# Performance work log

Hardware: AMD Instinct MI355X
Metric: run time of the kernel (lower is better)

## Reference

```python
import jax, jax.numpy as jnp
import numpy as np

# module hyperparameters (init kwargs)
D_MODEL = 1024
NUM_HEADS = 16
D_K = D_MODEL // NUM_HEADS
WINDOW_SIZE = 256
GLOBAL_TOKENS = 64
SEQ_LEN = 4096
BATCH = 1
NEG_INF = float('-inf')


def build_local_window_mask(seq_len, window_size, global_tokens):
    # 0 where attention is allowed, -inf where blocked
    i = jnp.arange(seq_len)[:, None]
    j = jnp.arange(seq_len)[None, :]
    allowed = (i < global_tokens) | (j < global_tokens) | (jnp.abs(i - j) <= window_size)
    return jnp.where(allowed, 0.0, NEG_INF).astype(jnp.float32)


def setup_inputs() -> dict:
    key = jax.random.key(0)
    ks = jax.random.split(key, 12)
    s = 1.0 / np.sqrt(D_MODEL)
    inp = {
        'q': jax.random.normal(ks[0], (BATCH, SEQ_LEN, D_MODEL), jnp.float32),
        'k': jax.random.normal(ks[1], (BATCH, SEQ_LEN, D_MODEL), jnp.float32),
        'v': jax.random.normal(ks[2], (BATCH, SEQ_LEN, D_MODEL), jnp.float32),
        # nn.Linear weights: shape (out, in), applied as x @ W.T + b
        'w_q': jax.random.normal(ks[3], (D_MODEL, D_MODEL), jnp.float32) * s,
        'b_q': jax.random.normal(ks[4], (D_MODEL,), jnp.float32) * s,
        'w_k': jax.random.normal(ks[5], (D_MODEL, D_MODEL), jnp.float32) * s,
        'b_k': jax.random.normal(ks[6], (D_MODEL,), jnp.float32) * s,
        'w_v': jax.random.normal(ks[7], (D_MODEL, D_MODEL), jnp.float32) * s,
        'b_v': jax.random.normal(ks[8], (D_MODEL,), jnp.float32) * s,
        'w_o': jax.random.normal(ks[9], (D_MODEL, D_MODEL), jnp.float32) * s,
        'b_o': jax.random.normal(ks[10], (D_MODEL,), jnp.float32) * s,
    }
    return inp


def reference(q, k, v, w_q, b_q, w_k, b_k, w_v, b_v, w_o, b_o):
    B, S, _ = q.shape
    scale = 1.0 / np.sqrt(D_K)

    def proj(x, w, b):  # (B,S,D) -> (B,H,S,Dk)
        y = x @ w.T + b
        return y.reshape(B, S, NUM_HEADS, D_K).transpose(0, 2, 1, 3)

    Q = proj(q, w_q, b_q)
    K = proj(k, w_k, b_k)
    V = proj(v, w_v, b_v)

    local_mask = build_local_window_mask(S, WINDOW_SIZE, GLOBAL_TOKENS)  # (S,S)
    scores = jnp.einsum('bhqd,bhkd->bhqk', Q, K) * scale + local_mask[None, None]
    attn = jax.nn.softmax(scores, axis=-1)
    out = jnp.einsum('bhqk,bhkd->bhqd', attn, V)  # (B,H,S,Dk)
    out = out.transpose(0, 2, 1, 3).reshape(B, S, D_MODEL)
    return out @ w_o.T + b_o
```

## Files before the change

kernel.cpp:

```cpp
#include <hip/hip_runtime.h>

#define S_LEN 4096
#define DMODEL 1024
#define NHEADS 16
#define DKH 64
#define WIN 256
#define GTOK 64
#define NSPLIT 8

typedef unsigned short u16t;
typedef __attribute__((ext_vector_type(8))) short short8;
typedef __attribute__((ext_vector_type(4))) float f32x4;

__device__ __forceinline__ u16t f2bf(float x) {
  union { float f; unsigned int u; } v; v.f = x;
  unsigned int r = v.u + 0x7FFFu + ((v.u >> 16) & 1u);
  return (u16t)(r >> 16);
}

__device__ __forceinline__ unsigned int cvtpk(float lo, float hi) {
  unsigned int r;
  asm("v_cvt_pk_bf16_f32 %0, %1, %2" : "=v"(r) : "v"(lo), "v"(hi));
  return r;
}

__device__ __forceinline__ void gload_lds16(const u16t* g, u16t* l) {
  __builtin_amdgcn_global_load_lds(
      (const __attribute__((address_space(1))) void*)g,
      (__attribute__((address_space(3))) void*)l, 16, 0, 0);
}

__global__ void cvt_all(const float* __restrict__ s0, const float* __restrict__ s1,
                        const float* __restrict__ s2, const float* __restrict__ s3,
                        const float* __restrict__ s4, const float* __restrict__ s5,
                        const float* __restrict__ s6,
                        u16t* __restrict__ d0, u16t* __restrict__ d1,
                        u16t* __restrict__ d2, u16t* __restrict__ d3,
                        u16t* __restrict__ d4, u16t* __restrict__ d5,
                        u16t* __restrict__ d6) {
  size_t i = (size_t)blockIdx.x * 1024 + threadIdx.x * 4;
  const float* s; u16t* d; size_t local;
  if (i < ((size_t)4 << 20)) {
    int which = (int)(i >> 20);
    local = i & ((1u << 20) - 1);
    s = which == 0 ? s0 : which == 1 ? s1 : which == 2 ? s2 : s3;
    d = which == 0 ? d0 : which == 1 ? d1 : which == 2 ? d2 : d3;
  } else {
    size_t j = i - ((size_t)4 << 20);
    int which = (int)(j >> 22);
    local = j & ((1u << 22) - 1);
    s = which == 0 ? s4 : which == 1 ? s5 : s6;
    d = which == 0 ? d4 : which == 1 ? d5 : d6;
  }
  float4 f = *(const float4*)(s + local);
  unsigned int lo = (unsigned int)f2bf(f.x) | ((unsigned int)f2bf(f.y) << 16);
  unsigned int hi = (unsigned int)f2bf(f.z) | ((unsigned int)f2bf(f.w) << 16);
  *(uint2*)(d + local) = make_uint2(lo, hi);
}

#define BN 128
#define GBK 64

template<int OUT_F32, int BMT, int BIAS_ROW>
__device__ __forceinline__
void gemm_body(u16t* __restrict__ sA, u16t* __restrict__ sB,
               const u16t* __restrict__ A, const u16t* __restrict__ B,
               const float* __restrict__ bias, void* __restrict__ Y,
               int N, int K, float alpha, int m0, int n0)
{
  constexpr int MF = BMT / 32;
  constexpr int CA_ISS = BMT * 2 / 64;

  const int tid = threadIdx.x;
  const int lane = tid & 63;
  const int lr = lane & 15, lg = lane >> 4;
  const int w = tid >> 6;
  const int wm = (w >> 1) * (MF * 16), wn = (w & 1) * 64;

  f32x4 acc[MF][4] = {};
  const int nk = K / GBK;

  for (int kt = 0; kt < nk; ++kt) {
    if (kt) __syncthreads();
#pragma unroll
    for (int i = 0; i < CA_ISS; ++i) {
      int c0 = w * (BMT * 2) + i * 64;
      int c = c0 + lane;
      int row = c >> 3, g = (c & 7) ^ (row & 7);
      gload_lds16(A + (size_t)(m0 + row) * K + kt * GBK + g * 8, sA + (size_t)c0 * 8);
    }
#pragma unroll
    for (int i = 0; i < 4; ++i) {
      int c0 = w * 256 + i * 64;
      int c = c0 + lane;
      int row = c >> 3, g = (c & 7) ^ (row & 7);
      gload_lds16(B + (size_t)(n0 + row) * K + kt * GBK + g * 8, sB + (size_t)c0 * 8);
    }
    __syncthreads();

    short8 af[MF][2], bf[4][2];
#pragma unroll
    for (int mf = 0; mf < MF; ++mf)
#pragma unroll
      for (int kk = 0; kk < 2; ++kk) {
        int s = ((kk * 4 + lg) ^ (lr & 7));
        af[mf][kk] = *(const short8*)&sA[(wm + mf * 16 + lr) * GBK + s * 8];
      }
#pragma unroll
    for (int nf = 0; nf < 4; ++nf)
#pragma unroll
      for (int kk = 0; kk < 2; ++kk) {
        int s = ((kk * 4 + lg) ^ (lr & 7));
        bf[nf][kk] = *(const short8*)&sB[(wn + nf * 16 + lr) * GBK + s * 8];
      }
    __builtin_amdgcn_s_setprio(1);
#pragma unroll
    for (int kk = 0; kk < 2; ++kk)
#pragma unroll
      for (int mf = 0; mf < MF; ++mf)
#pragma unroll
        for (int nf = 0; nf < 4; ++nf)
          acc[mf][nf] = __builtin_amdgcn_mfma_f32_16x16x32_bf16(af[mf][kk], bf[nf][kk], acc[mf][nf], 0, 0, 0);
    __builtin_amdgcn_s_setprio(0);
  }

#pragma unroll
  for (int nf = 0; nf < 4; ++nf) {
    int col = n0 + wn + nf * 16 + lr;
    float bvc = BIAS_ROW ? 0.f : bias[col];
#pragma unroll
    for (int mf = 0; mf < MF; ++mf)
#pragma unroll
      for (int r = 0; r < 4; ++r) {
        int row = m0 + wm + mf * 16 + lg * 4 + r;
        float bv = BIAS_ROW ? bias[row] : bvc;
        float v = (acc[mf][nf][r] + bv) * alpha;
        if (OUT_F32) ((float*)Y)[(size_t)row * N + col] = v;
        else         ((u16t*)Y)[(size_t)row * N + col] = f2bf(v);
      }
  }
}

#define QSCALE 0.18033688011112042f
__global__ __launch_bounds__(256)
void gemm_qkv(const u16t* __restrict__ xq, const u16t* __restrict__ xk, const u16t* __restrict__ xv,
              const u16t* __restrict__ wq, const u16t* __restrict__ wk, const u16t* __restrict__ wv,
              const float* __restrict__ bq, const float* __restrict__ bk, const float* __restrict__ bv,
              u16t* __restrict__ Qp, u16t* __restrict__ Kp, u16t* __restrict__ Vt)
{
  __shared__ __align__(16) u16t smem[2 * 128 * GBK];
  u16t* sA = smem;
  u16t* sB = smem + 128 * GBK;

  int b = blockIdx.x;
  int wid = (b & 7) * 96 + (b >> 3);
  int z = wid >> 8;
  int rem = wid & 255;
  if (z == 0) {
    gemm_body<0, 128, 0>(sA, sB, xq, wq, bq, Qp, DMODEL, DMODEL, QSCALE, (rem >> 3) * 128, (rem & 7) * BN);
  } else if (z == 1) {
    gemm_body<0, 128, 0>(sA, sB, xk, wk, bk, Kp, DMODEL, DMODEL, 1.0f, (rem >> 3) * 128, (rem & 7) * BN);
  } else {
    gemm_body<0, 128, 1>(sA, sB, wv, xv, bv, Vt, S_LEN, DMODEL, 1.0f, (rem & 7) * 128, (rem >> 3) * BN);
  }
}

__global__ __launch_bounds__(256)
void gemm_o(const u16t* __restrict__ A, const u16t* __restrict__ B,
            const float* __restrict__ bias, float* __restrict__ Y)
{
  __shared__ __align__(16) u16t smem[(64 + 128) * GBK];
  u16t* sA = smem;
  u16t* sB = smem + 64 * GBK;

  int b = blockIdx.x;
  int wid = (b & 7) * 64 + (b >> 3);
  int my = wid >> 3, mx = wid & 7;
  gemm_body<1, 64, 0>(sA, sB, A, B, bias, Y, DMODEL, DMODEL, 1.0f, my * 64, mx * BN);
}

__global__ __launch_bounds__(256)
void attn_kernel(const u16t* __restrict__ Qp, const u16t* __restrict__ Kp,
                 const u16t* __restrict__ Vt, u16t* __restrict__ AO,
                 float* __restrict__ pacc, float* __restrict__ pml)
{
  __shared__ __align__(16) u16t sK[2][64 * 64];
  __shared__ __align__(16) u16t sV[2][64 * 64];
  __shared__ __align__(16) u16t sP[4][16 * 64];

  const int b = blockIdx.x;
  const int wid = (b & 7) * 142 + (b >> 3);
  const int h = wid / 71;
  const int x = wid % 71;

  const int tid = threadIdx.x, w = tid >> 6, lane = tid & 63;
  const int lr = lane & 15, lg = lane >> 4;

  const bool windowed = (x < 63);
  const int qb = windowed ? (x + 1) : 0;
  const int split = windowed ? 0 : (x - 63);
  const int qw = qb * 64 + w * 16;

  short8 qf[2];
#pragma unroll
  for (int kk = 0; kk < 2; ++kk)
    qf[kk] = *(const short8*)(Qp + (size_t)(qw + lr) * DMODEL + h * DKH + kk * 32 + lg * 8);

  f32x4 acc[4] = {};
  float m_run = -1e30f;
  float l_run = 0.f;

  int lo = 1, nkv;
  if (windowed) {
    lo = (qb - 4 < 1) ? 1 : qb - 4;
    int hi = (qb + 4 > 63) ? 63 : qb + 4;
    nkv = hi - lo + 2;
  } else {
    nkv = 64 / NSPLIT;
  }

#define KVB(idx) (windowed ? ((idx) == 0 ? 0 : lo + (idx) - 1) : (split * (64 / NSPLIT) + (idx)))

  auto stage = [&](int buf, int kvb) {
    int kv0 = kvb * 64;
#pragma unroll
    for (int j = 0; j < 2; ++j) {
      int c = tid + j * 256;
      int row = c >> 3, g = (c & 7) ^ (row & 7);
      gload_lds16(Kp + (size_t)(kv0 + row) * DMODEL + h * DKH + g * 8, &sK[buf][c * 8]);
    }
#pragma unroll
    for (int j = 0; j < 2; ++j) {
      int c = tid + j * 256;
      int row = c >> 3, g = (c & 7) ^ (row & 7);
      gload_lds16(Vt + (size_t)(h * DKH + row) * S_LEN + kv0 + g * 8, &sV[buf][c * 8]);
    }
  };

  stage(0, KVB(0));
  __syncthreads();

  for (int idx = 0; idx < nkv; ++idx) {
    const int buf = idx & 1;
    const int kvb = KVB(idx);
    const int kv0 = kvb * 64;

    if (idx + 1 < nkv) stage(buf ^ 1, KVB(idx + 1));

    f32x4 sacc[4] = {};
    __builtin_amdgcn_s_setprio(1);
#pragma unroll
    for (int kk = 0; kk < 2; ++kk)
#pragma unroll
      for (int nf = 0; nf < 4; ++nf) {
        int s = ((kk * 4 + lg) ^ (lr & 7));
        short8 kf = *(const short8*)&sK[buf][(nf * 16 + lr) * 64 + s * 8];
        sacc[nf] = __builtin_amdgcn_mfma_f32_16x16x32_bf16(kf, qf[kk], sacc[nf], 0, 0, 0);
      }
    __builtin_amdgcn_s_setprio(0);

    if (windowed && (kvb == qb + 4 || (kvb == qb - 4 && kvb > 0))) {
      int qg = qw + lr;
#pragma unroll
      for (int nf = 0; nf < 4; ++nf)
#pragma unroll
        for (int r = 0; r < 4; ++r) {
          int sg = kv0 + nf * 16 + lg * 4 + r;
          int diff = qg - sg; if (diff < 0) diff = -diff;
          if (diff > WIN) sacc[nf][r] = -1e30f;
        }
    }

    float rm0 = fmaxf(fmaxf(sacc[0][0], sacc[0][1]), sacc[0][2]);
    float rm1 = fmaxf(fmaxf(sacc[0][3], sacc[1][0]), sacc[1][1]);
    float rm2 = fmaxf(fmaxf(sacc[1][2], sacc[1][3]), sacc[2][0]);
    float rm3 = fmaxf(fmaxf(sacc[2][1], sacc[2][2]), sacc[2][3]);
    float rm4 = fmaxf(fmaxf(sacc[3][0], sacc[3][1]), sacc[3][2]);
    float rm = fmaxf(fmaxf(rm0, rm1), fmaxf(fmaxf(rm2, rm3), fmaxf(rm4, sacc[3][3])));

    if (!__all(rm <= m_run + 11.0f)) {
      rm = fmaxf(rm, __shfl_xor(rm, 16));
      rm = fmaxf(rm, __shfl_xor(rm, 32));
      float mnew = fmaxf(m_run, rm);
      float corr = exp2f(m_run - mnew);
      m_run = mnew;
      l_run *= corr;
      float cq[4];
#pragma unroll
      for (int r = 0; r < 4; ++r) cq[r] = __shfl(corr, lg * 4 + r);
#pragma unroll
      for (int nf = 0; nf < 4; ++nf)
#pragma unroll
        for (int r = 0; r < 4; ++r) acc[nf][r] *= cq[r];
    }

    float p[4][4];
    float rs = 0.f;
#pragma unroll
    for (int nf = 0; nf < 4; ++nf)
#pragma unroll
      for (int r = 0; r < 4; ++r) {
        float e = exp2f(sacc[nf][r] - m_run);
        p[nf][r] = e;
        rs += e;
      }
    l_run += rs;

#pragma unroll
    for (int nf = 0; nf < 4; ++nf) {
      unsigned int lo32 = cvtpk(p[nf][0], p[nf][1]);
      unsigned int hi32 = cvtpk(p[nf][2], p[nf][3]);
      int blk = (nf * 2 + (lg >> 1)) ^ (lr & 7);
      *(uint2*)&sP[w][lr * 64 + blk * 8 + (lg & 1) * 4] = make_uint2(lo32, hi32);
    }

#pragma unroll
    for (int kk = 0; kk < 2; ++kk) {
      short8 pf = *(const short8*)&sP[w][lr * 64 + (((kk * 4 + lg) ^ (lr & 7))) * 8];
      __builtin_amdgcn_s_setprio(1);
#pragma unroll
      for (int nf = 0; nf < 4; ++nf) {
        int s = ((kk * 4 + lg) ^ (lr & 7));
        short8 vf = *(const short8*)&sV[buf][(nf * 16 + lr) * 64 + s * 8];
        acc[nf] = __builtin_amdgcn_mfma_f32_16x16x32_bf16(pf, vf, acc[nf], 0, 0, 0);
      }
      __builtin_amdgcn_s_setprio(0);
    }

    if (idx + 1 < nkv) __syncthreads();
  }
#undef KVB

  l_run += __shfl_xor(l_run, 16);
  l_run += __shfl_xor(l_run, 32);

  if (windowed) {
    float lq[4];
#pragma unroll
    for (int r = 0; r < 4; ++r) lq[r] = __shfl(l_run, lg * 4 + r);
#pragma unroll
    for (int nf = 0; nf < 4; ++nf)
#pragma unroll
      for (int r = 0; r < 4; ++r) {
        float v = acc[nf][r] / lq[r];
        AO[(size_t)(qw + lg * 4 + r) * DMODEL + h * DKH + nf * 16 + lr] = f2bf(v);
      }
  } else {
    const int pbase = (h * NSPLIT + split) * 64;
#pragma unroll
    for (int nf = 0; nf < 4; ++nf)
#pragma unroll
      for (int r = 0; r < 4; ++r)
        pacc[(size_t)(pbase + w * 16 + lg * 4 + r) * 64 + nf * 16 + lr] = acc[nf][r];
    if (lane < 16) {
      int bb = (pbase + w * 16 + lane) * 2;
      pml[bb] = m_run;
      pml[bb + 1] = l_run;
    }
  }
}

__global__ __launch_bounds__(256)
void merge_kernel(const float* __restrict__ pacc, const float* __restrict__ pml,
                  u16t* __restrict__ AO)
{
  const int h = blockIdx.x;
  const int tid = threadIdx.x;
  const int row = tid >> 2;
  const int d0 = (tid & 3) * 16;

  float M = -1e30f;
#pragma unroll
  for (int s = 0; s < NSPLIT; ++s)
    M = fmaxf(M, pml[((h * NSPLIT + s) * 64 + row) * 2]);

  float L = 0.f;
  float o[16];
#pragma unroll
  for (int e = 0; e < 16; ++e) o[e] = 0.f;

#pragma unroll
  for (int s = 0; s < NSPLIT; ++s) {
    int b = ((h * NSPLIT + s) * 64 + row) * 2;
    float sc = exp2f(pml[b] - M);
    L += pml[b + 1] * sc;
    const float4* a = (const float4*)(pacc + ((size_t)(h * NSPLIT + s) * 64 + row) * 64 + d0);
#pragma unroll
    for (int q4 = 0; q4 < 4; ++q4) {
      float4 av = a[q4];
      o[q4 * 4 + 0] += av.x * sc;
      o[q4 * 4 + 1] += av.y * sc;
      o[q4 * 4 + 2] += av.z * sc;
      o[q4 * 4 + 3] += av.w * sc;
    }
  }
  float inv = 1.f / L;
#pragma unroll
  for (int e = 0; e < 16; ++e)
    AO[(size_t)row * DMODEL + h * DKH + d0 + e] = f2bf(o[e] * inv);
}

extern "C" void kernel_launch(void* const* d_in, const int* in_sizes, int n_in,
                              void* d_out, int out_size, void* d_ws, size_t ws_size,
                              hipStream_t stream) {
  const float* q   = (const float*)d_in[0];
  const float* k   = (const float*)d_in[1];
  const float* v   = (const float*)d_in[2];
  const float* w_q = (const float*)d_in[3];
  const float* b_q = (const float*)d_in[4];
  const float* w_k = (const float*)d_in[5];
  const float* b_k = (const float*)d_in[6];
  const float* w_v = (const float*)d_in[7];
  const float* b_v = (const float*)d_in[8];
  const float* w_o = (const float*)d_in[9];
  const float* b_o = (const float*)d_in[10];

  u16t* ws = (u16t*)d_ws;
  const size_t SZX = (size_t)S_LEN * DMODEL;
  const size_t SZW = (size_t)DMODEL * DMODEL;
  u16t* xq  = ws;
  u16t* xk  = xq + SZX;
  u16t* xv  = xk + SZX;
  u16t* wb0 = xv + SZX;
  u16t* wb1 = wb0 + SZW;
  u16t* wb2 = wb1 + SZW;
  u16t* wb3 = wb2 + SZW;
  u16t* Qp  = wb3 + SZW;
  u16t* Kp  = Qp + SZX;
  u16t* Vt  = Kp + SZX;
  u16t* AO  = xk;
  float* pacc = (float*)xq;
  float* pml  = pacc + (size_t)NHEADS * NSPLIT * 64 * 64;

  dim3 blk(256);

  cvt_all<<<(int)((4 * SZW + 3 * SZX) / 1024), blk, 0, stream>>>(
      w_q, w_k, w_v, w_o, q, k, v, wb0, wb1, wb2, wb3, xq, xk, xv);

  gemm_qkv<<<768, blk, 0, stream>>>(xq, xk, xv, wb0, wb1, wb2, b_q, b_k, b_v, Qp, Kp, Vt);

  attn_kernel<<<(63 + NSPLIT) * NHEADS, blk, 0, stream>>>(Qp, Kp, Vt, AO, pacc, pml);
  merge_kernel<<<NHEADS, blk, 0, stream>>>(pacc, pml, AO);

  gemm_o<<<512, blk, 0, stream>>>(AO, wb3, b_o, (float*)d_out);
}
```

Measured before the change: 112.1 us.

## Double-buffer LDS tiles in the QKV and output projection GEMMs

The shared GEMM body now keeps two LDS tile buffers. It issues the global-to-LDS loads for the next K tile before running the MFMAs on the current one, so copy latency can hide behind compute. This drops one barrier per iteration. In exchange, each GEMM block uses twice as much LDS, which may lower how many blocks fit on a compute unit.

Result: no change. 110.0 us (median of 3 runs) (-1.8%).

```diff
diff --git a/kernel.cpp b/kernel.cpp
--- a/kernel.cpp
+++ b/kernel.cpp
@@ -63,13 +63,14 @@
 
 template<int OUT_F32, int BMT, int BIAS_ROW>
 __device__ __forceinline__
-void gemm_body(u16t* __restrict__ sA, u16t* __restrict__ sB,
+void gemm_body(u16t* __restrict__ smem,
                const u16t* __restrict__ A, const u16t* __restrict__ B,
                const float* __restrict__ bias, void* __restrict__ Y,
                int N, int K, float alpha, int m0, int n0)
 {
   constexpr int MF = BMT / 32;
   constexpr int CA_ISS = BMT * 2 / 64;
+  constexpr int TILE = (BMT + BN) * GBK;
 
   const int tid = threadIdx.x;
   const int lane = tid & 63;
@@ -80,8 +81,9 @@
   f32x4 acc[MF][4] = {};
   const int nk = K / GBK;
 
-  for (int kt = 0; kt < nk; ++kt) {
-    if (kt) __syncthreads();
+  auto stage = [&](int buf, int kt) {
+    u16t* sA = smem + buf * TILE;
+    u16t* sB = sA + BMT * GBK;
 #pragma unroll
     for (int i = 0; i < CA_ISS; ++i) {
       int c0 = w * (BMT * 2) + i * 64;
@@ -96,7 +98,17 @@
       int row = c >> 3, g = (c & 7) ^ (row & 7);
       gload_lds16(B + (size_t)(n0 + row) * K + kt * GBK + g * 8, sB + (size_t)c0 * 8);
     }
-    __syncthreads();
+  };
+
+  stage(0, 0);
+  __syncthreads();
+
+  for (int kt = 0; kt < nk; ++kt) {
+    const int buf = kt & 1;
+    if (kt + 1 < nk) stage(buf ^ 1, kt + 1);
+
+    const u16t* sA = smem + buf * TILE;
+    const u16t* sB = sA + BMT * GBK;
 
     short8 af[MF][2], bf[4][2];
 #pragma unroll
@@ -122,6 +134,8 @@
         for (int nf = 0; nf < 4; ++nf)
           acc[mf][nf] = __builtin_amdgcn_mfma_f32_16x16x32_bf16(af[mf][kk], bf[nf][kk], acc[mf][nf], 0, 0, 0);
     __builtin_amdgcn_s_setprio(0);
+
+    if (kt + 1 < nk) __syncthreads();
   }
 
 #pragma unroll
@@ -148,20 +162,18 @@
               const float* __restrict__ bq, const float* __restrict__ bk, const float* __restrict__ bv,
               u16t* __restrict__ Qp, u16t* __restrict__ Kp, u16t* __restrict__ Vt)
 {
-  __shared__ __align__(16) u16t smem[2 * 128 * GBK];
-  u16t* sA = smem;
-  u16t* sB = smem + 128 * GBK;
+  __shared__ __align__(16) u16t smem[2 * (128 + 128) * GBK];
 
   int b = blockIdx.x;
   int wid = (b & 7) * 96 + (b >> 3);
   int z = wid >> 8;
   int rem = wid & 255;
   if (z == 0) {
-    gemm_body<0, 128, 0>(sA, sB, xq, wq, bq, Qp, DMODEL, DMODEL, QSCALE, (rem >> 3) * 128, (rem & 7) * BN);
+    gemm_body<0, 128, 0>(smem, xq, wq, bq, Qp, DMODEL, DMODEL, QSCALE, (rem >> 3) * 128, (rem & 7) * BN);
   } else if (z == 1) {
-    gemm_body<0, 128, 0>(sA, sB, xk, wk, bk, Kp, DMODEL, DMODEL, 1.0f, (rem >> 3) * 128, (rem & 7) * BN);
+    gemm_body<0, 128, 0>(smem, xk, wk, bk, Kp, DMODEL, DMODEL, 1.0f, (rem >> 3) * 128, (rem & 7) * BN);
   } else {
-    gemm_body<0, 128, 1>(sA, sB, wv, xv, bv, Vt, S_LEN, DMODEL, 1.0f, (rem & 7) * 128, (rem >> 3) * BN);
+    gemm_body<0, 128, 1>(smem, wv, xv, bv, Vt, S_LEN, DMODEL, 1.0f, (rem & 7) * 128, (rem >> 3) * BN);
   }
 }
 
@@ -169,14 +181,12 @@
 void gemm_o(const u16t* __restrict__ A, const u16t* __restrict__ B,
             const float* __restrict__ bias, float* __restrict__ Y)
 {
-  __shared__ __align__(16) u16t smem[(64 + 128) * GBK];
-  u16t* sA = smem;
-  u16t* sB = smem + 64 * GBK;
+  __shared__ __align__(16) u16t smem[2 * (64 + 128) * GBK];
 
   int b = blockIdx.x;
   int wid = (b & 7) * 64 + (b >> 3);
   int my = wid >> 3, mx = wid & 7;
-  gemm_body<1, 64, 0>(sA, sB, A, B, bias, Y, DMODEL, DMODEL, 1.0f, my * 64, mx * BN);
+  gemm_body<1, 64, 0>(smem, A, B, bias, Y, DMODEL, DMODEL, 1.0f, my * 64, mx * BN);
 }
 
 __global__ __launch_bounds__(256)
```
